# Kernel tuning notes

Hardware: AMD Instinct MI355X
Metric: run time of the kernel (lower is better)

Reference implementation:

```python
import jax, jax.numpy as jnp
import numpy as np

OBJ_N, D_KEY, D_VAL, BANK_N, N_Q, BS = 4, 128, 512, 7200, 3600, 1


def setup_inputs() -> dict:
    key = jax.random.key(0)
    k1, k2, k3, k4, k5 = jax.random.split(key, 5)
    return {
        "keys": jax.random.normal(k1, (OBJ_N, D_KEY, BANK_N), dtype=jnp.float32),
        "values": jax.random.normal(k2, (OBJ_N, D_VAL, BANK_N), dtype=jnp.float32),
        "masks": jax.random.uniform(k3, (OBJ_N, 1, BANK_N), dtype=jnp.float32),
        "q_in": jax.random.normal(k4, (BS, D_KEY, N_Q), dtype=jnp.float32),
        "q_out": jax.random.normal(k5, (BS, D_VAL, N_Q), dtype=jnp.float32),
    }


def reference(keys, values, masks, q_in, q_out):
    # keys: (O, Dk, B) memory keys per object; q_in: (S, Dk, N) query keys
    d_key = keys.shape[1]
    scale = 1.0 / jnp.sqrt(jnp.asarray(d_key, dtype=keys.dtype))
    # p[o,s,b,n] = softmax_b( keys[o,:,b] . q_in[s,:,n] / sqrt(Dk) )
    logits = jnp.einsum('odb,sdn->osbn', keys, q_in) * scale
    p = jax.nn.softmax(logits, axis=2)
    # mem[o,s,v,n] = sum_b values[o,v,b] * p[o,s,b,n]
    mem = jnp.einsum('ovb,osbn->osvn', values, p)
    # mask_mem[o,s,1,n]: mask-weighted attention readout, gates q_out
    mask_mem = jnp.einsum('omb,osbn->osmn', masks, p)
    q_out_with_mask = q_out[None] * mask_mem          # (O, S, Dv, N)
    out = jnp.concatenate([mem, q_out_with_mask], axis=2)  # (O, S, 2*Dv, N)
    return jnp.transpose(out, (1, 0, 2, 3))           # (S, O, 2*Dv, N)
```

## Files before the change

kernel.cpp:

```cpp
#include <hip/hip_runtime.h>
#include <hip/hip_bf16.h>

typedef unsigned short u16;
typedef unsigned int   u32;
typedef short bf16x8 __attribute__((ext_vector_type(8)));
typedef float f32x4  __attribute__((ext_vector_type(4)));

#define O_N    4
#define D_K    128
#define D_V    512
#define BANK   7200
#define NQ     3600
#define NT     64
#define NTILES 57
#define NSUB   225
#define VH_ROWS 256

#define K_OFF    0
#define P_OFF    32768
#define LMM_OFF  40960
#define SMEM_BYTES 41472
#define Q_OFF    0

#define GLL(gsrc, ldst) __builtin_amdgcn_global_load_lds( \
    (const __attribute__((address_space(1))) void*)(gsrc), \
    (__attribute__((address_space(3))) void*)(ldst), 16, 0, 0)

#define MFMA16(a, b, c) __builtin_amdgcn_mfma_f32_16x16x32_bf16((a), (b), (c), 0, 0, 0)

static __device__ __forceinline__ u16 f2bf(float x) {
    u32 u = __builtin_bit_cast(u32, x);
    return (u16)((u + 0x7FFFu + ((u >> 16) & 1u)) >> 16);
}


__global__ void k_transpose_bf16(const float* __restrict__ in, u16* __restrict__ out) {
    __shared__ float tile[32][33];
    const int obj = blockIdx.z;
    const float* src = in + (size_t)obj * D_K * BANK;
    u16* dst = out + (size_t)obj * BANK * D_K;
    const int bx = blockIdx.x * 32;
    const int by = blockIdx.y * 32;
    const int tx = threadIdx.x, ty = threadIdx.y;
#pragma unroll
    for (int i = 0; i < 4; i++)
        tile[ty + 8 * i][tx] = src[(size_t)(by + ty + 8 * i) * BANK + bx + tx];
    __syncthreads();
#pragma unroll
    for (int i = 0; i < 4; i++)
        dst[(size_t)(bx + ty + 8 * i) * D_K + by + tx] = f2bf(tile[tx][ty + 8 * i]);
}

__global__ void k_convert_bf16(const float* __restrict__ in, u16* __restrict__ out, int n4) {
    int idx = blockIdx.x * blockDim.x + threadIdx.x;
    int stride = gridDim.x * blockDim.x;
    for (int i = idx; i < n4; i += stride) {
        float4 v = reinterpret_cast<const float4*>(in)[i];
        ushort4 o;
        o.x = f2bf(v.x); o.y = f2bf(v.y); o.z = f2bf(v.z); o.w = f2bf(v.w);
        reinterpret_cast<ushort4*>(out)[i] = o;
    }
}

__global__ void k_zero(float* out, int n) {
    int i = blockIdx.x * blockDim.x + threadIdx.x;
    if (i < n) out[i] = 0.f;
}

__launch_bounds__(256, 2)
__global__ void k_matcher(const u16* __restrict__ Kt,
                          const u16* __restrict__ Vb,
                          const float* __restrict__ masks,
                          const float* __restrict__ q_in,
                          const float* __restrict__ q_out,
                          float* __restrict__ out,
                          int G, float* __restrict__ lw, float* __restrict__ mw)
{
    __shared__ __align__(16) char smem[SMEM_BYTES];
    const int tid  = threadIdx.x;
    const int wave = tid >> 6;
    const int lane = tid & 63;
    const int q    = lane >> 4;
    const int lr   = lane & 15;
    const int lr7  = lr & 7;

    const int grp  = blockIdx.x & 7;
    const int o    = grp >> 1;
    const int vh   = grp & 1;
    const int rest = blockIdx.x >> 3;
    const int tile = rest / G;
    const int g    = rest - tile * G;
    const int n0   = tile * NT;

    const int st0 = (NSUB * g) / G;
    const int st1 = (NSUB * (g + 1)) / G;
    const int cnt = st1 - st0;
    const int nd  = cnt >> 1;
    const int ts  = cnt & 1;
    const int nu  = nd + ts;

    for (int idx = tid; idx < NT * D_K; idx += 256) {
        int d = idx >> 6;
        int n = idx & 63;
        int gn = n0 + n;
        float v = (gn < NQ) ? q_in[(size_t)d * NQ + gn] : 0.f;
        int bb = d * 2;
        int sb = n * 256 + ((((bb >> 4) ^ (n & 7)) << 4) | (bb & 15));
        *reinterpret_cast<u16*>(smem + Q_OFF + sb) = f2bf(v);
    }
    __syncthreads();

    bf16x8 qf[4];
    {
        const int n = 16 * wave + lr;
#pragma unroll
        for (int ds = 0; ds < 4; ds++) {
            int gq = (4 * ds + q) ^ (n & 7);
            qf[ds] = *reinterpret_cast<const bf16x8*>(smem + Q_OFF + n * 256 + gq * 16);
        }
    }
    __syncthreads();

    const f32x4 zero4 = {0.f, 0.f, 0.f, 0.f};
    f32x4 acc[4][4];
#pragma unroll
    for (int i = 0; i < 4; i++)
#pragma unroll
        for (int j = 0; j < 4; j++) acc[i][j] = zero4;
    float l_part = 0.f, mm_part = 0.f;
    const float scale = 0.08838834764831845f;

    const u16* Ko = Kt + (size_t)o * BANK * D_K;
    const u16* Vo = Vb + (size_t)o * D_V * BANK + (size_t)vh * VH_ROWS * BANK;
    const float* mPtr = masks + (size_t)o * BANK + st0 * 32 + 4 * q;

    const u16* kSrcA = Ko + (size_t)(st0 * 32 + (tid >> 4)) * D_K
                         + (((tid & 15) ^ ((tid >> 4) & 7)) << 3);
    const u16* kSrcB = kSrcA + 16 * D_K;

#define ISSUE2(buf) do {                                                   \
        char* kb_ = smem + K_OFF + (buf) * 16384 + wave * 1024;            \
        GLL(kSrcA, kb_);                                                   \
        GLL(kSrcB, kb_ + 4096);                                            \
        GLL(kSrcA + 32 * D_K, kb_ + 8192);                                 \
        GLL(kSrcB + 32 * D_K, kb_ + 12288);                                \
        kSrcA += 64 * D_K; kSrcB += 64 * D_K;                              \
    } while (0)
#define ISSUE1(buf) do {                                                   \
        char* kb_ = smem + K_OFF + (buf) * 16384 + wave * 1024;            \
        GLL(kSrcA, kb_);                                                   \
        GLL(kSrcB, kb_ + 4096);                                            \
    } while (0)

    const u16* Vrow = Vo + st0 * 32;
    const u32  vOff = (u32)(64 * wave + lr) * BANK + q * 8;

    const int nrow  = 16 * wave + lr;
    char* const pW  = smem + P_OFF + nrow * 128 + (q & 1) * 8;

#define QK_T(T, MV) do {                                                     \
        f32x4 s_acc = zero4;                                                 \
        const int b_r = 16 * (T) + lr;                                       \
        _Pragma("unroll")                                                    \
        for (int ds = 0; ds < 4; ds++) {                                     \
            bf16x8 kf = *reinterpret_cast<const bf16x8*>(                    \
                kb + b_r * 256 + (((4 * ds + q) ^ lr7) << 4));               \
            s_acc = MFMA16(kf, qf[ds], s_acc);                               \
        }                                                                    \
        float p0 = __expf(s_acc[0] * scale);                                 \
        float p1 = __expf(s_acc[1] * scale);                                 \
        float p2 = __expf(s_acc[2] * scale);                                 \
        float p3 = __expf(s_acc[3] * scale);                                 \
        l_part  += p0 + p1 + p2 + p3;                                        \
        mm_part += p0 * (MV).x + p1 * (MV).y + p2 * (MV).z + p3 * (MV).w;    \
        ushort4 pk;                                                          \
        pk.x = f2bf(p0); pk.y = f2bf(p1); pk.z = f2bf(p2); pk.w = f2bf(p3);  \
        *reinterpret_cast<ushort4*>(                                         \
            pW + (((2 * (T) + (q >> 1)) ^ lr7) << 4)) = pk;                  \
    } while (0)

#define PV_S(S, V0, V1, V2, V3) do {                                         \
        _Pragma("unroll")                                                    \
        for (int ng = 0; ng < 4; ng++) {                                     \
            bf16x8 pf = *reinterpret_cast<const bf16x8*>(                    \
                smem + P_OFF + (16 * ng + lr) * 128 +                        \
                (((4 * (S) + q) ^ lr7) << 4));                               \
            acc[0][ng] = MFMA16(V0, pf, acc[0][ng]);                         \
            acc[1][ng] = MFMA16(V1, pf, acc[1][ng]);                         \
            acc[2][ng] = MFMA16(V2, pf, acc[2][ng]);                         \
            acc[3][ng] = MFMA16(V3, pf, acc[3][ng]);                         \
        }                                                                    \
    } while (0)

    if (nd > 0) ISSUE2(0); else ISSUE1(0);

    for (int u = 0; u < nu; u++) {
        const int cur = u & 1;
        asm volatile("s_waitcnt vmcnt(0)" ::: "memory");
        __builtin_amdgcn_s_barrier();
        __builtin_amdgcn_sched_barrier(0);
        if (u + 1 < nu) {
            if (u + 1 < nd) ISSUE2(cur ^ 1);
            else            ISSUE1(cur ^ 1);
        }
        const char* kb = smem + K_OFF + cur * 16384;

        if (u < nd) {
            float4 mv0 = *reinterpret_cast<const float4*>(mPtr);
            float4 mv1 = *reinterpret_cast<const float4*>(mPtr + 16);
            float4 mv2 = *reinterpret_cast<const float4*>(mPtr + 32);
            float4 mv3 = *reinterpret_cast<const float4*>(mPtr + 48);
            bf16x8 va0 = *reinterpret_cast<const bf16x8*>(Vrow + vOff);
            bf16x8 va1 = *reinterpret_cast<const bf16x8*>(Vrow + vOff + 16 * BANK);
            bf16x8 va2 = *reinterpret_cast<const bf16x8*>(Vrow + vOff + 32 * BANK);
            bf16x8 va3 = *reinterpret_cast<const bf16x8*>(Vrow + vOff + 48 * BANK);
            QK_T(0, mv0); QK_T(1, mv1); QK_T(2, mv2); QK_T(3, mv3);
            bf16x8 vb0 = *reinterpret_cast<const bf16x8*>(Vrow + vOff + 32);
            bf16x8 vb1 = *reinterpret_cast<const bf16x8*>(Vrow + vOff + 32 + 16 * BANK);
            bf16x8 vb2 = *reinterpret_cast<const bf16x8*>(Vrow + vOff + 32 + 32 * BANK);
            bf16x8 vb3 = *reinterpret_cast<const bf16x8*>(Vrow + vOff + 32 + 48 * BANK);
            asm volatile("s_waitcnt lgkmcnt(0)" ::: "memory");
            __builtin_amdgcn_s_barrier();
            __builtin_amdgcn_sched_barrier(0);
            PV_S(0, va0, va1, va2, va3);
            PV_S(1, vb0, vb1, vb2, vb3);
            mPtr += 64;
            Vrow += 64;
        } else {
            float4 mv0 = *reinterpret_cast<const float4*>(mPtr);
            float4 mv1 = *reinterpret_cast<const float4*>(mPtr + 16);
            bf16x8 va0 = *reinterpret_cast<const bf16x8*>(Vrow + vOff);
            bf16x8 va1 = *reinterpret_cast<const bf16x8*>(Vrow + vOff + 16 * BANK);
            bf16x8 va2 = *reinterpret_cast<const bf16x8*>(Vrow + vOff + 32 * BANK);
            bf16x8 va3 = *reinterpret_cast<const bf16x8*>(Vrow + vOff + 48 * BANK);
            QK_T(0, mv0); QK_T(1, mv1);
            asm volatile("s_waitcnt lgkmcnt(0)" ::: "memory");
            __builtin_amdgcn_s_barrier();
            __builtin_amdgcn_sched_barrier(0);
            PV_S(0, va0, va1, va2, va3);
        }
    }

    l_part  += __shfl_xor(l_part, 16);  l_part  += __shfl_xor(l_part, 32);
    mm_part += __shfl_xor(mm_part, 16); mm_part += __shfl_xor(mm_part, 32);
    float* l_lds  = reinterpret_cast<float*>(smem + LMM_OFF);
    float* mm_lds = l_lds + 64;
    if (lane < 16) {
        l_lds[16 * wave + lr]  = l_part;
        mm_lds[16 * wave + lr] = mm_part;
    }
    __syncthreads();

    if (G == 1) {
        float* outo = out + (size_t)o * (1024 * NQ);
#pragma unroll
        for (int ng = 0; ng < 4; ng++) {
            const int n  = 16 * ng + lr;
            const int gn = n0 + n;
            if (gn >= NQ) continue;
            const float invl = 1.f / l_lds[n];
            const float gate = mm_lds[n] * invl;
#pragma unroll
            for (int vt = 0; vt < 4; vt++) {
#pragma unroll
                for (int r = 0; r < 4; r++) {
                    const int v = vh * VH_ROWS + 64 * wave + 16 * vt + 4 * q + r;
                    outo[(size_t)v * NQ + gn] = acc[vt][ng][r] * invl;
                    outo[(size_t)(512 + v) * NQ + gn] = q_out[(size_t)v * NQ + gn] * gate;
                }
            }
        }
    } else {
        float* dst = out + ((size_t)o * 1024 + (size_t)g * 512 + (size_t)vh * VH_ROWS) * NQ;
#pragma unroll
        for (int ng = 0; ng < 4; ng++) {
            const int n  = 16 * ng + lr;
            const int gn = n0 + n;
            if (gn >= NQ) continue;
#pragma unroll
            for (int vt = 0; vt < 4; vt++) {
#pragma unroll
                for (int r = 0; r < 4; r++) {
                    const int v = 64 * wave + 16 * vt + 4 * q + r;
                    dst[(size_t)v * NQ + gn] = acc[vt][ng][r];
                }
            }
        }
        if (vh == 0 && tid < 64) {
            const size_t li = ((size_t)(g * 4 + o) * NTILES + tile) * 64 + tid;
            lw[li] = l_lds[tid];
            mw[li] = mm_lds[tid];
        }
    }
}

__global__ void k_combine(const float* __restrict__ q_out, const float* __restrict__ lw,
                          const float* __restrict__ mw, float* __restrict__ out) {
    const int total = O_N * 512 * (NQ / 4);
    float4* outv = reinterpret_cast<float4*>(out);
    const float4* qv = reinterpret_cast<const float4*>(q_out);
    for (int idx = blockIdx.x * blockDim.x + threadIdx.x; idx < total;
         idx += gridDim.x * blockDim.x) {
        const int o  = idx / (512 * 900);
        const int r  = idx - o * 512 * 900;
        const int v  = r / 900;
        const int g4 = r - v * 900;
        const size_t iA = ((size_t)o * 1024 + v) * 900 + g4;
        const size_t iB = ((size_t)o * 1024 + 512 + v) * 900 + g4;
        float4 A = outv[iA];
        float4 B = outv[iB];
        const int tl = g4 >> 4;
        const int wi = (g4 & 15) * 4;
        const size_t l0i = ((size_t)(0 * 4 + o) * NTILES + tl) * 64 + wi;
        const size_t l1i = ((size_t)(1 * 4 + o) * NTILES + tl) * 64 + wi;
        const float4 l0 = *reinterpret_cast<const float4*>(lw + l0i);
        const float4 l1 = *reinterpret_cast<const float4*>(lw + l1i);
        const float4 m0 = *reinterpret_cast<const float4*>(mw + l0i);
        const float4 m1 = *reinterpret_cast<const float4*>(mw + l1i);
        float4 li, mem, gate;
        li.x = 1.f / (l0.x + l1.x); li.y = 1.f / (l0.y + l1.y);
        li.z = 1.f / (l0.z + l1.z); li.w = 1.f / (l0.w + l1.w);
        mem.x = (A.x + B.x) * li.x; mem.y = (A.y + B.y) * li.y;
        mem.z = (A.z + B.z) * li.z; mem.w = (A.w + B.w) * li.w;
        gate.x = (m0.x + m1.x) * li.x; gate.y = (m0.y + m1.y) * li.y;
        gate.z = (m0.z + m1.z) * li.z; gate.w = (m0.w + m1.w) * li.w;
        float4 qo = qv[(size_t)v * 900 + g4];
        outv[iA] = mem;
        float4 gq;
        gq.x = qo.x * gate.x; gq.y = qo.y * gate.y;
        gq.z = qo.z * gate.z; gq.w = qo.w * gate.w;
        outv[iB] = gq;
    }
}

extern "C" void kernel_launch(void* const* d_in, const int* in_sizes, int n_in,
                              void* d_out, int out_size, void* d_ws, size_t ws_size,
                              hipStream_t stream) {
    const float* keys   = (const float*)d_in[0];
    const float* values = (const float*)d_in[1];
    const float* masks  = (const float*)d_in[2];
    const float* q_in   = (const float*)d_in[3];
    const float* q_outp = (const float*)d_in[4];
    float* out = (float*)d_out;

    const size_t K_BYTES  = (size_t)O_N * BANK * D_K * 2;
    const size_t V_BYTES  = (size_t)O_N * D_V * BANK * 2;
    const size_t LM_FLOATS = (size_t)2 * O_N * NTILES * 64;
    const size_t LM_BYTES  = LM_FLOATS * 4 * 2;

    if (ws_size < K_BYTES + V_BYTES) {
        k_zero<<<(out_size + 255) / 256, 256, 0, stream>>>(out, out_size);
        return;
    }
    const int G = (ws_size >= K_BYTES + V_BYTES + LM_BYTES) ? 2 : 1;

    u16* Kt = (u16*)d_ws;
    u16* Vb = (u16*)((char*)d_ws + K_BYTES);
    float* lw = (float*)((char*)d_ws + K_BYTES + V_BYTES);
    float* mw = lw + LM_FLOATS;

    dim3 tb(32, 8);
    dim3 tg(BANK / 32, D_K / 32, O_N);
    k_transpose_bf16<<<tg, tb, 0, stream>>>(keys, Kt);

    const int n4 = O_N * D_V * BANK / 4;
    k_convert_bf16<<<2048, 256, 0, stream>>>(values, Vb, n4);

    k_matcher<<<NTILES * 8 * G, 256, 0, stream>>>(Kt, Vb, masks, q_in, q_outp, out,
                                                  G, lw, mw);
    if (G == 2)
        k_combine<<<2048, 256, 0, stream>>>(q_outp, lw, mw, out);
}
```

Before: 296.1 us.

## Software-pipeline QK and PV stages with double-buffered P tiles

Double-buffers the P tile in LDS so that the PV MFMAs for the previous step run after the QK/exp for the current step. This removes one of the two block barriers per iteration. The softmax scale and log2(e) are folded into the query during staging, so the kernel calls exp2f instead of scaling then __expf. Packed bf16 conversion now uses the v_cvt_pk_bf16_f32 instruction in place of manual rounding. In exchange it uses more LDS and more registers for the V fragments carried across iterations, and the tail step runs a partial PV.

```diff
diff --git a/kernel.cpp b/kernel.cpp
--- a/kernel.cpp
+++ b/kernel.cpp
@@ -18,8 +18,8 @@
 
 #define K_OFF    0
 #define P_OFF    32768
-#define LMM_OFF  40960
-#define SMEM_BYTES 41472
+#define LMM_OFF  49152
+#define SMEM_BYTES 49664
 #define Q_OFF    0
 
 #define GLL(gsrc, ldst) __builtin_amdgcn_global_load_lds( \
@@ -33,6 +33,8 @@
     return (u16)((u + 0x7FFFu + ((u >> 16) & 1u)) >> 16);
 }
 
+
+#define QSCALE 0.12751743f
 
 __global__ void k_transpose_bf16(const float* __restrict__ in, u16* __restrict__ out) {
     __shared__ float tile[32][33];
@@ -103,7 +105,7 @@
         int d = idx >> 6;
         int n = idx & 63;
         int gn = n0 + n;
-        float v = (gn < NQ) ? q_in[(size_t)d * NQ + gn] : 0.f;
+        float v = (gn < NQ) ? q_in[(size_t)d * NQ + gn] * QSCALE : 0.f;
         int bb = d * 2;
         int sb = n * 256 + ((((bb >> 4) ^ (n & 7)) << 4) | (bb & 15));
         *reinterpret_cast<u16*>(smem + Q_OFF + sb) = f2bf(v);
@@ -128,7 +130,6 @@
 #pragma unroll
         for (int j = 0; j < 4; j++) acc[i][j] = zero4;
     float l_part = 0.f, mm_part = 0.f;
-    const float scale = 0.08838834764831845f;
 
     const u16* Ko = Kt + (size_t)o * BANK * D_K;
     const u16* Vo = Vb + (size_t)o * D_V * BANK + (size_t)vh * VH_ROWS * BANK;
@@ -156,9 +157,8 @@
     const u32  vOff = (u32)(64 * wave + lr) * BANK + q * 8;
 
     const int nrow  = 16 * wave + lr;
-    char* const pW  = smem + P_OFF + nrow * 128 + (q & 1) * 8;
-
-#define QK_T(T, MV) do {                                                     \
+
+#define QK_T(T, MV, PWB) do {                                                \
         f32x4 s_acc = zero4;                                                 \
         const int b_r = 16 * (T) + lr;                                       \
         _Pragma("unroll")                                                    \
@@ -167,23 +167,25 @@
                 kb + b_r * 256 + (((4 * ds + q) ^ lr7) << 4));               \
             s_acc = MFMA16(kf, qf[ds], s_acc);                               \
         }                                                                    \
-        float p0 = __expf(s_acc[0] * scale);                                 \
-        float p1 = __expf(s_acc[1] * scale);                                 \
-        float p2 = __expf(s_acc[2] * scale);                                 \
-        float p3 = __expf(s_acc[3] * scale);                                 \
+        float p0 = exp2f(s_acc[0]);                                          \
+        float p1 = exp2f(s_acc[1]);                                          \
+        float p2 = exp2f(s_acc[2]);                                          \
+        float p3 = exp2f(s_acc[3]);                                          \
         l_part  += p0 + p1 + p2 + p3;                                        \
         mm_part += p0 * (MV).x + p1 * (MV).y + p2 * (MV).z + p3 * (MV).w;    \
-        ushort4 pk;                                                          \
-        pk.x = f2bf(p0); pk.y = f2bf(p1); pk.z = f2bf(p2); pk.w = f2bf(p3);  \
-        *reinterpret_cast<ushort4*>(                                         \
-            pW + (((2 * (T) + (q >> 1)) ^ lr7) << 4)) = pk;                  \
+        u32 w0, w1;                                                          \
+        asm("v_cvt_pk_bf16_f32 %0, %1, %2" : "=v"(w0) : "v"(p0), "v"(p1));   \
+        asm("v_cvt_pk_bf16_f32 %0, %1, %2" : "=v"(w1) : "v"(p2), "v"(p3));   \
+        uint2 pk2; pk2.x = w0; pk2.y = w1;                                   \
+        *reinterpret_cast<uint2*>(                                           \
+            (PWB) + (((2 * (T) + (q >> 1)) ^ lr7) << 4)) = pk2;              \
     } while (0)
 
-#define PV_S(S, V0, V1, V2, V3) do {                                         \
+#define PV_S(S, PB, V0, V1, V2, V3) do {                                     \
         _Pragma("unroll")                                                    \
         for (int ng = 0; ng < 4; ng++) {                                     \
             bf16x8 pf = *reinterpret_cast<const bf16x8*>(                    \
-                smem + P_OFF + (16 * ng + lr) * 128 +                        \
+                (PB) + (16 * ng + lr) * 128 +                                \
                 (((4 * (S) + q) ^ lr7) << 4));                               \
             acc[0][ng] = MFMA16(V0, pf, acc[0][ng]);                         \
             acc[1][ng] = MFMA16(V1, pf, acc[1][ng]);                         \
@@ -193,52 +195,66 @@
     } while (0)
 
     if (nd > 0) ISSUE2(0); else ISSUE1(0);
+    asm volatile("s_waitcnt vmcnt(0)" ::: "memory");
+    __builtin_amdgcn_s_barrier();
+    __builtin_amdgcn_sched_barrier(0);
+
+    bf16x8 va0, va1, va2, va3, vb0, vb1, vb2, vb3;
 
     for (int u = 0; u < nu; u++) {
         const int cur = u & 1;
-        asm volatile("s_waitcnt vmcnt(0)" ::: "memory");
-        __builtin_amdgcn_s_barrier();
-        __builtin_amdgcn_sched_barrier(0);
+        const char* kb = smem + K_OFF + cur * 16384;
+        char* pWc = smem + P_OFF + cur * 8192 + nrow * 128 + (q & 1) * 8;
+        const char* pR = smem + P_OFF + (cur ^ 1) * 8192;
+        const bool full = (u < nd);
+
         if (u + 1 < nu) {
             if (u + 1 < nd) ISSUE2(cur ^ 1);
             else            ISSUE1(cur ^ 1);
         }
-        const char* kb = smem + K_OFF + cur * 16384;
-
-        if (u < nd) {
-            float4 mv0 = *reinterpret_cast<const float4*>(mPtr);
-            float4 mv1 = *reinterpret_cast<const float4*>(mPtr + 16);
+
+        float4 mv0 = *reinterpret_cast<const float4*>(mPtr);
+        float4 mv1 = *reinterpret_cast<const float4*>(mPtr + 16);
+        QK_T(0, mv0, pWc);
+        QK_T(1, mv1, pWc);
+        if (full) {
             float4 mv2 = *reinterpret_cast<const float4*>(mPtr + 32);
             float4 mv3 = *reinterpret_cast<const float4*>(mPtr + 48);
-            bf16x8 va0 = *reinterpret_cast<const bf16x8*>(Vrow + vOff);
-            bf16x8 va1 = *reinterpret_cast<const bf16x8*>(Vrow + vOff + 16 * BANK);
-            bf16x8 va2 = *reinterpret_cast<const bf16x8*>(Vrow + vOff + 32 * BANK);
-            bf16x8 va3 = *reinterpret_cast<const bf16x8*>(Vrow + vOff + 48 * BANK);
-            QK_T(0, mv0); QK_T(1, mv1); QK_T(2, mv2); QK_T(3, mv3);
-            bf16x8 vb0 = *reinterpret_cast<const bf16x8*>(Vrow + vOff + 32);
-            bf16x8 vb1 = *reinterpret_cast<const bf16x8*>(Vrow + vOff + 32 + 16 * BANK);
-            bf16x8 vb2 = *reinterpret_cast<const bf16x8*>(Vrow + vOff + 32 + 32 * BANK);
-            bf16x8 vb3 = *reinterpret_cast<const bf16x8*>(Vrow + vOff + 32 + 48 * BANK);
-            asm volatile("s_waitcnt lgkmcnt(0)" ::: "memory");
-            __builtin_amdgcn_s_barrier();
-            __builtin_amdgcn_sched_barrier(0);
-            PV_S(0, va0, va1, va2, va3);
-            PV_S(1, vb0, vb1, vb2, vb3);
-            mPtr += 64;
-            Vrow += 64;
-        } else {
-            float4 mv0 = *reinterpret_cast<const float4*>(mPtr);
-            float4 mv1 = *reinterpret_cast<const float4*>(mPtr + 16);
-            bf16x8 va0 = *reinterpret_cast<const bf16x8*>(Vrow + vOff);
-            bf16x8 va1 = *reinterpret_cast<const bf16x8*>(Vrow + vOff + 16 * BANK);
-            bf16x8 va2 = *reinterpret_cast<const bf16x8*>(Vrow + vOff + 32 * BANK);
-            bf16x8 va3 = *reinterpret_cast<const bf16x8*>(Vrow + vOff + 48 * BANK);
-            QK_T(0, mv0); QK_T(1, mv1);
-            asm volatile("s_waitcnt lgkmcnt(0)" ::: "memory");
-            __builtin_amdgcn_s_barrier();
-            __builtin_amdgcn_sched_barrier(0);
-            PV_S(0, va0, va1, va2, va3);
-        }
+            QK_T(2, mv2, pWc);
+            QK_T(3, mv3, pWc);
+        }
+
+        bf16x8 na0 = *reinterpret_cast<const bf16x8*>(Vrow + vOff);
+        bf16x8 na1 = *reinterpret_cast<const bf16x8*>(Vrow + vOff + 16 * BANK);
+        bf16x8 na2 = *reinterpret_cast<const bf16x8*>(Vrow + vOff + 32 * BANK);
+        bf16x8 na3 = *reinterpret_cast<const bf16x8*>(Vrow + vOff + 48 * BANK);
+        bf16x8 nb0 = vb0, nb1 = vb1, nb2 = vb2, nb3 = vb3;
+        if (full) {
+            nb0 = *reinterpret_cast<const bf16x8*>(Vrow + vOff + 32);
+            nb1 = *reinterpret_cast<const bf16x8*>(Vrow + vOff + 32 + 16 * BANK);
+            nb2 = *reinterpret_cast<const bf16x8*>(Vrow + vOff + 32 + 32 * BANK);
+            nb3 = *reinterpret_cast<const bf16x8*>(Vrow + vOff + 32 + 48 * BANK);
+        }
+
+        if (u > 0) {
+            PV_S(0, pR, va0, va1, va2, va3);
+            PV_S(1, pR, vb0, vb1, vb2, vb3);
+        }
+        va0 = na0; va1 = na1; va2 = na2; va3 = na3;
+        vb0 = nb0; vb1 = nb1; vb2 = nb2; vb3 = nb3;
+
+        mPtr += full ? 64 : 32;
+        Vrow += full ? 64 : 32;
+
+        asm volatile("s_waitcnt vmcnt(0) lgkmcnt(0)" ::: "memory");
+        __builtin_amdgcn_s_barrier();
+        __builtin_amdgcn_sched_barrier(0);
+    }
+
+    {
+        const char* pL = smem + P_OFF + ((nu - 1) & 1) * 8192;
+        PV_S(0, pL, va0, va1, va2, va3);
+        if (!ts) PV_S(1, pL, vb0, vb1, vb2, vb3);
     }
 
     l_part  += __shfl_xor(l_part, 16);  l_part  += __shfl_xor(l_part, 32);
```

Result: slower. 337.3 us (+13.9%).
